# Performance work log

Measured on AMD Instinct MI355X. Metric: run time of the kernel, lower is better.

## Reference

```python
import jax, jax.numpy as jnp
import numpy as np

B, C, H, W = 4, 256, 64, 64
CK = C // 8  # query/key channels per OUT_RATIO=8


def setup_inputs() -> dict:
    key = jax.random.key(0)
    ks = jax.random.split(key, 8)
    s_in = 1.0 / np.sqrt(C)
    return {
        "x": jax.random.normal(ks[0], (B, C, H, W), dtype=jnp.float32),
        "Wq": jax.random.uniform(ks[1], (CK, C), jnp.float32, -s_in, s_in),
        "bq": jax.random.uniform(ks[2], (CK,), jnp.float32, -s_in, s_in),
        "Wk": jax.random.uniform(ks[3], (CK, C), jnp.float32, -s_in, s_in),
        "bk": jax.random.uniform(ks[4], (CK,), jnp.float32, -s_in, s_in),
        "Wv": jax.random.uniform(ks[5], (C, C), jnp.float32, -s_in, s_in),
        "bv": jax.random.uniform(ks[6], (C,), jnp.float32, -s_in, s_in),
        "gamma": jnp.zeros((1,), dtype=jnp.float32),
    }


def reference(x, Wq, bq, Wk, bk, Wv, bv, gamma):
    b, c, h, w = x.shape
    n = h * w
    xf = x.reshape(b, c, n)  # [B, C, N]
    # 1x1 convs are channel matmuls
    q = jnp.einsum('oc,bcn->bno', Wq, xf) + bq  # [B, N, CK]
    k = jnp.einsum('oc,bcn->bon', Wk, xf) + bk[None, :, None]  # [B, CK, N]
    v = jnp.einsum('oc,bcn->bon', Wv, xf) + bv[None, :, None]  # [B, C, N]
    energy = jnp.einsum('bno,bom->bnm', q, k)  # [B, N, N], unscaled
    attn = jax.nn.softmax(energy, axis=-1)
    out = jnp.einsum('bcm,bnm->bcn', v, attn)  # [B, C, N]
    out = out.reshape(b, c, h, w)
    return gamma[0] * out + x
```

## Files before the change

kernel.cpp:

```cpp
#include <hip/hip_runtime.h>
#include <math.h>


#define BB 4
#define CC 256
#define NN 4096
#define CKK 32
#define LOG2E 1.44269504f

typedef __attribute__((ext_vector_type(4))) float f32x4;
typedef __attribute__((ext_vector_type(16))) float f32x16;
typedef __attribute__((ext_vector_type(8))) short short8;
typedef __attribute__((ext_vector_type(4))) short short4v;

static __device__ __forceinline__ ushort f2bf(float f) {
    union { float f; unsigned u; } v; v.f = f;
    unsigned r = v.u + 0x7FFFu + ((v.u >> 16) & 1u);
    return (ushort)(r >> 16);
}
static __device__ __forceinline__ float bf2f(ushort h) {
    union { unsigned u; float f; } v; v.u = ((unsigned)h) << 16;
    return v.f;
}
static __device__ __forceinline__ unsigned pack2(float lo, float hi) {
    unsigned r;
    asm("v_cvt_pk_bf16_f32 %0, %1, %2" : "=v"(r) : "v"(lo), "v"(hi));
    return r;
}
static __device__ __forceinline__ float exp2fast(float x) {
    return __builtin_amdgcn_exp2f(x);
}

#define VSEL(chunk, c) (((chunk) * 1024) + ((((c) ^ (((chunk) >> 1) << 2))) << 2))

__global__ __launch_bounds__(256) void pack_w_kernel(
    const float* __restrict__ Wq, const float* __restrict__ bq,
    const float* __restrict__ Wk, const float* __restrict__ bk,
    const float* __restrict__ Wv, const float* __restrict__ bv,
    ushort* __restrict__ Wb, float* __restrict__ bias)
{
    const int o = blockIdx.x;
    const int c = threadIdx.x;
    const float* src; float bsc;
    if (o < 32)      { src = Wq + o * CC;        bsc = bq[o]; }
    else if (o < 64) { src = Wk + (o - 32) * CC; bsc = bk[o - 32]; }
    else             { src = Wv + (o - 64) * CC; bsc = bv[o - 64]; }
    Wb[o * CC + c] = f2bf(src[c]);
    if (c == 0) bias[o] = bsc;
}

__global__ __launch_bounds__(256) void xpose_kernel(
    const float* __restrict__ x, ushort* __restrict__ xT)
{
    __shared__ float t[32][33];
    const int b = blockIdx.z, c0 = blockIdx.y * 32, n0 = blockIdx.x * 32;
    const int tid = threadIdx.x;
    #pragma unroll
    for (int i = 0; i < 4; ++i) {
        int idx = tid + i * 256, rr = idx >> 5, nn = idx & 31;
        t[rr][nn] = x[((size_t)b * CC + c0 + rr) * NN + n0 + nn];
    }
    __syncthreads();
    #pragma unroll
    for (int i = 0; i < 4; ++i) {
        int idx = tid + i * 256, rr = idx >> 5, cc = idx & 31;
        xT[((size_t)b * NN + n0 + rr) * CC + c0 + cc] = f2bf(t[cc][rr]);
    }
}

__global__ __launch_bounds__(256) void qkv_mfma_kernel(
    const ushort* __restrict__ Wb, const float* __restrict__ bias,
    const ushort* __restrict__ xT,
    ushort* __restrict__ Q, ushort* __restrict__ Kt, ushort* __restrict__ V)
{
    const int b = blockIdx.y, n0 = blockIdx.x * 64;
    const int tid = threadIdx.x;
    const int w = tid >> 6, lane = tid & 63, l15 = lane & 15, q = lane >> 4;

    f32x4 acc[5][4];
    #pragma unroll
    for (int c5 = 0; c5 < 5; ++c5)
        #pragma unroll
        for (int nc = 0; nc < 4; ++nc) acc[c5][nc] = (f32x4)0.f;

    #pragma unroll
    for (int ks = 0; ks < 8; ++ks) {
        short8 af[5], bf[4];
        #pragma unroll
        for (int c5 = 0; c5 < 5; ++c5)
            af[c5] = *(const short8*)&Wb[(w * 80 + c5 * 16 + l15) * CC + ks * 32 + q * 8];
        #pragma unroll
        for (int nc = 0; nc < 4; ++nc)
            bf[nc] = *(const short8*)&xT[((size_t)b * NN + n0 + nc * 16 + l15) * CC + ks * 32 + q * 8];
        #pragma unroll
        for (int c5 = 0; c5 < 5; ++c5)
            #pragma unroll
            for (int nc = 0; nc < 4; ++nc)
                acc[c5][nc] = __builtin_amdgcn_mfma_f32_16x16x32_bf16(af[c5], bf[nc], acc[c5][nc], 0, 0, 0);
    }

    #pragma unroll
    for (int c5 = 0; c5 < 5; ++c5) {
        const int o0 = w * 80 + c5 * 16;
        float bia[4];
        #pragma unroll
        for (int r = 0; r < 4; ++r) bia[r] = bias[o0 + q * 4 + r];
        if (o0 >= 64) {
            #pragma unroll
            for (int nc = 0; nc < 4; ++nc)
                #pragma unroll
                for (int r = 0; r < 4; ++r)
                    V[((size_t)b * CC + o0 - 64 + q * 4 + r) * NN + n0 + nc * 16 + l15] =
                        f2bf(acc[c5][nc][r] + bia[r]);
        } else {
            ushort* dst = (o0 < 32) ? Q : Kt;
            const float sc = (o0 < 32) ? LOG2E : 1.0f;
            const int oo = (o0 & 31) + q * 4;
            #pragma unroll
            for (int nc = 0; nc < 4; ++nc) {
                short4v h;
                #pragma unroll
                for (int r = 0; r < 4; ++r) h[r] = (short)f2bf((acc[c5][nc][r] + bia[r]) * sc);
                *(short4v*)&dst[((size_t)b * NN + n0 + nc * 16 + l15) * CKK + oo] = h;
            }
        }
    }
}

__global__ __launch_bounds__(256, 2) void attn_mfma_kernel(
    const ushort* __restrict__ Q, const ushort* __restrict__ K,
    const ushort* __restrict__ V,
    ushort* __restrict__ Op, float* __restrict__ Mp, float* __restrict__ Lp,
    int G, int NSEG)
{
    __shared__ __align__(16) ushort vs2[2][8192];

    const int id = blockIdx.x;
    const int xcd = id & 7, ix = id >> 3;
    const int b = xcd >> 1;
    int g, row;
    if (G == 4) { g = ((xcd & 1) << 1) | (ix & 1); row = ix >> 1; }
    else        { g = xcd & 1;                     row = ix; }
    const int n0 = row * 128;

    const int tid = threadIdx.x;
    const int w = tid >> 6, lane = tid & 63;
    const int l31 = lane & 31, h2 = lane >> 5;
    const int n0w = n0 + w * 32;

    const size_t qrow = ((size_t)b * NN + n0w + l31) * CKK;
    short8 qB0 = *(const short8*)&Q[qrow + h2 * 8];
    short8 qB1 = *(const short8*)&Q[qrow + 16 + h2 * 8];

    f32x16 acc[8];
    #pragma unroll
    for (int cb = 0; cb < 8; ++cb) acc[cb] = (f32x16)0.f;
    float m_i = -3.0e38f, l_p = 0.f;

    const size_t kgb = (size_t)b * NN * CKK;
    const size_t vgb = (size_t)b * CC * NN;
    const int m_start = g * NSEG;
    const int NT = NSEG / 32;

    const int srow = tid >> 2, sseg = tid & 3;

    short8 kA0 = *(const short8*)&K[kgb + (size_t)(m_start + l31) * CKK + h2 * 8];
    short8 kA1 = *(const short8*)&K[kgb + (size_t)(m_start + l31) * CKK + 16 + h2 * 8];
    union { short8 v; short4v h[2]; } vr[4];
    #pragma unroll
    for (int i = 0; i < 4; ++i)
        vr[i].v = *(const short8*)&V[vgb + (size_t)(srow + i * 64) * NN + m_start + sseg * 8];
    #pragma unroll
    for (int i = 0; i < 4; ++i) {
        const int c = srow + i * 64;
        *(short4v*)&vs2[0][VSEL(2 * sseg,     c)] = vr[i].h[0];
        *(short4v*)&vs2[0][VSEL(2 * sseg + 1, c)] = vr[i].h[1];
    }
    __syncthreads();

    int cur = 0;
    for (int mt = 0; mt < NT; ++mt) {
        const bool more = (mt + 1 < NT);
        const int m0n = more ? m_start + (mt + 1) * 32 : m_start;

        f32x16 s = __builtin_amdgcn_mfma_f32_32x32x16_bf16(kA0, qB0, (f32x16)0.f, 0, 0, 0);
        s = __builtin_amdgcn_mfma_f32_32x32x16_bf16(kA1, qB1, s, 0, 0, 0);

        kA0 = *(const short8*)&K[kgb + (size_t)(m0n + l31) * CKK + h2 * 8];
        kA1 = *(const short8*)&K[kgb + (size_t)(m0n + l31) * CKK + 16 + h2 * 8];
        #pragma unroll
        for (int i = 0; i < 4; ++i)
            vr[i].v = *(const short8*)&V[vgb + (size_t)(srow + i * 64) * NN + m0n + sseg * 8];

        float mx = fmaxf(
            fmaxf(fmaxf(fmaxf(s[0], s[1]), fmaxf(s[2], s[3])),
                  fmaxf(fmaxf(s[4], s[5]), fmaxf(s[6], s[7]))),
            fmaxf(fmaxf(fmaxf(s[8], s[9]), fmaxf(s[10], s[11])),
                  fmaxf(fmaxf(s[12], s[13]), fmaxf(s[14], s[15]))));
        mx = fmaxf(mx, __shfl_xor(mx, 32));
        const bool resc = mx > m_i + 8.f;
        const float mn = resc ? mx : m_i;
        const float al = resc ? exp2fast(m_i - mx) : 1.f;
        float pp[16];
        #pragma unroll
        for (int r = 0; r < 16; ++r) pp[r] = exp2fast(s[r] - mn);
        float sum = ((pp[0] + pp[1]) + (pp[2] + pp[3])) + ((pp[4] + pp[5]) + (pp[6] + pp[7]))
                  + ((pp[8] + pp[9]) + (pp[10] + pp[11])) + ((pp[12] + pp[13]) + (pp[14] + pp[15]));
        l_p = l_p * al + sum;
        m_i = mn;
        if (__any(resc)) {
            #pragma unroll
            for (int cb = 0; cb < 8; ++cb) acc[cb] *= al;
        }

        union { unsigned u[8]; short8 v[2]; } P;
        #pragma unroll
        for (int g2 = 0; g2 < 8; ++g2) P.u[g2] = pack2(pp[2 * g2], pp[2 * g2 + 1]);

        __builtin_amdgcn_s_setprio(1);
        #pragma unroll
        for (int cb = 0; cb < 8; ++cb) {
            const int c = cb * 32 + l31;
            union { short4v h[2]; short8 v; } A0, A1;
            A0.h[0] = *(const short4v*)&vs2[cur][VSEL(h2,     c)];
            A0.h[1] = *(const short4v*)&vs2[cur][VSEL(2 + h2, c)];
            A1.h[0] = *(const short4v*)&vs2[cur][VSEL(4 + h2, c)];
            A1.h[1] = *(const short4v*)&vs2[cur][VSEL(6 + h2, c)];
            acc[cb] = __builtin_amdgcn_mfma_f32_32x32x16_bf16(A0.v, P.v[0], acc[cb], 0, 0, 0);
            acc[cb] = __builtin_amdgcn_mfma_f32_32x32x16_bf16(A1.v, P.v[1], acc[cb], 0, 0, 0);
        }
        __builtin_amdgcn_s_setprio(0);

        #pragma unroll
        for (int i = 0; i < 4; ++i) {
            const int c = srow + i * 64;
            *(short4v*)&vs2[cur ^ 1][VSEL(2 * sseg,     c)] = vr[i].h[0];
            *(short4v*)&vs2[cur ^ 1][VSEL(2 * sseg + 1, c)] = vr[i].h[1];
        }
        __syncthreads();
        cur ^= 1;
    }

    float l = l_p + __shfl_xor(l_p, 32);
    const float linv = 1.f / l;
    if (h2 == 0) {
        const size_t idx = (size_t)(g * BB + b) * NN + n0w + l31;
        Mp[idx] = m_i;
        Lp[idx] = l;
    }
    ushort* ob = Op + (size_t)(g * BB + b) * CC * NN;
    #pragma unroll
    for (int cb = 0; cb < 8; ++cb)
        #pragma unroll
        for (int r = 0; r < 16; ++r) {
            const int c = cb * 32 + (r & 3) + 8 * (r >> 2) + 4 * h2;
            ob[(size_t)c * NN + n0w + l31] = f2bf(acc[cb][r] * linv);
        }
}

template<int G>
__global__ __launch_bounds__(256) void combine_kernel(
    const ushort* __restrict__ Op, const float* __restrict__ Mp,
    const float* __restrict__ Lp, const float* __restrict__ x,
    const float* __restrict__ gamma, float* __restrict__ out)
{
    const int gid = blockIdx.x * 256 + threadIdx.x;
    const int grp   = gid & (NN / 8 - 1);
    const int rowid = gid >> 9;
    const int b = rowid >> 8;
    const int c = rowid & (CC - 1);
    const int n0 = grp * 8;

    f32x4 mp[G][2], lp[G][2];
    #pragma unroll
    for (int g = 0; g < G; ++g) {
        const size_t base = (size_t)(g * BB + b) * NN + n0;
        mp[g][0] = *(const f32x4*)&Mp[base];
        mp[g][1] = *(const f32x4*)&Mp[base + 4];
        lp[g][0] = *(const f32x4*)&Lp[base];
        lp[g][1] = *(const f32x4*)&Lp[base + 4];
    }
    float wgt[G][8];
    #pragma unroll
    for (int h = 0; h < 2; ++h) {
        #pragma unroll
        for (int j = 0; j < 4; ++j) {
            float M = -3.0e38f;
            #pragma unroll
            for (int g = 0; g < G; ++g) M = fmaxf(M, mp[g][h][j]);
            float ws = 0.f;
            #pragma unroll
            for (int g = 0; g < G; ++g) {
                const float wv = lp[g][h][j] * exp2fast(mp[g][h][j] - M);
                wgt[g][h * 4 + j] = wv;
                ws += wv;
            }
            const float inv = 1.f / ws;
            #pragma unroll
            for (int g = 0; g < G; ++g) wgt[g][h * 4 + j] *= inv;
        }
    }

    short8 opv[G];
    #pragma unroll
    for (int g = 0; g < G; ++g)
        opv[g] = *(const short8*)&Op[((size_t)(g * BB + b) * CC + c) * NN + n0];

    const size_t xbase = ((size_t)b * CC + c) * NN + n0;
    const f32x4 x0 = *(const f32x4*)&x[xbase];
    const f32x4 x1 = *(const f32x4*)&x[xbase + 4];
    const float gm = gamma[0];

    f32x4 o0, o1;
    #pragma unroll
    for (int j = 0; j < 4; ++j) {
        float a = 0.f, bsum = 0.f;
        #pragma unroll
        for (int g = 0; g < G; ++g) {
            a    += wgt[g][j]     * bf2f((ushort)opv[g][j]);
            bsum += wgt[g][4 + j] * bf2f((ushort)opv[g][4 + j]);
        }
        o0[j] = gm * a + x0[j];
        o1[j] = gm * bsum + x1[j];
    }
    *(f32x4*)&out[xbase]     = o0;
    *(f32x4*)&out[xbase + 4] = o1;
}

extern "C" void kernel_launch(void* const* d_in, const int* in_sizes, int n_in,
                              void* d_out, int out_size, void* d_ws, size_t ws_size,
                              hipStream_t stream) {
    const float* x     = (const float*)d_in[0];
    const float* Wq    = (const float*)d_in[1];
    const float* bq    = (const float*)d_in[2];
    const float* Wk    = (const float*)d_in[3];
    const float* bk    = (const float*)d_in[4];
    const float* Wv    = (const float*)d_in[5];
    const float* bv    = (const float*)d_in[6];
    const float* gamma = (const float*)d_in[7];
    float* out = (float*)d_out;

    char* p = (char*)d_ws;
    ushort* Wb   = (ushort*)(p);
    float*  bias = (float*) (p + 163840);
    ushort* xT   = (ushort*)(p + 165120);
    ushort* Qb   = (ushort*)(p + 8553728);
    ushort* Kb   = (ushort*)(p + 9602304);
    ushort* Vc   = (ushort*)(p + 10650880);
    float*  Mpb  = (float*) (p + 19039488);
    float*  Lpb  = (float*) (p + 19301632);
    ushort* Opb  = (ushort*)(p + 19563776);
    const int G = (ws_size >= (size_t)53118208) ? 4 : 2;

    pack_w_kernel<<<dim3(320), 256, 0, stream>>>(Wq, bq, Wk, bk, Wv, bv, Wb, bias);
    xpose_kernel<<<dim3(NN / 32, CC / 32, BB), 256, 0, stream>>>(x, xT);
    qkv_mfma_kernel<<<dim3(NN / 64, BB), 256, 0, stream>>>(Wb, bias, xT, Qb, Kb, Vc);
    attn_mfma_kernel<<<dim3(128 * G), 256, 0, stream>>>(Qb, Kb, Vc, Opb, Mpb, Lpb, G, NN / G);
    const int cblocks = BB * CC * (NN / 8) / 256;
    if (G == 4)
        combine_kernel<4><<<dim3(cblocks), 256, 0, stream>>>(Opb, Mpb, Lpb, x, gamma, out);
    else
        combine_kernel<2><<<dim3(cblocks), 256, 0, stream>>>(Opb, Mpb, Lpb, x, gamma, out);
}
```

Baseline: 97.24 us.

## Fuse transpose into QKV projection and software-pipeline QK^T in attention loop

Result: faster. 89.34 us (-8.1%).

```diff
diff --git a/kernel.cpp b/kernel.cpp
--- a/kernel.cpp
+++ b/kernel.cpp
@@ -30,8 +30,6 @@
 static __device__ __forceinline__ float exp2fast(float x) {
     return __builtin_amdgcn_exp2f(x);
 }
-
-#define VSEL(chunk, c) (((chunk) * 1024) + ((((c) ^ (((chunk) >> 1) << 2))) << 2))
 
 __global__ __launch_bounds__(256) void pack_w_kernel(
     const float* __restrict__ Wq, const float* __restrict__ bq,
@@ -49,28 +47,9 @@
     if (c == 0) bias[o] = bsc;
 }
 
-__global__ __launch_bounds__(256) void xpose_kernel(
-    const float* __restrict__ x, ushort* __restrict__ xT)
-{
-    __shared__ float t[32][33];
-    const int b = blockIdx.z, c0 = blockIdx.y * 32, n0 = blockIdx.x * 32;
-    const int tid = threadIdx.x;
-    #pragma unroll
-    for (int i = 0; i < 4; ++i) {
-        int idx = tid + i * 256, rr = idx >> 5, nn = idx & 31;
-        t[rr][nn] = x[((size_t)b * CC + c0 + rr) * NN + n0 + nn];
-    }
-    __syncthreads();
-    #pragma unroll
-    for (int i = 0; i < 4; ++i) {
-        int idx = tid + i * 256, rr = idx >> 5, cc = idx & 31;
-        xT[((size_t)b * NN + n0 + rr) * CC + c0 + cc] = f2bf(t[cc][rr]);
-    }
-}
-
 __global__ __launch_bounds__(256) void qkv_mfma_kernel(
     const ushort* __restrict__ Wb, const float* __restrict__ bias,
-    const ushort* __restrict__ xT,
+    const float* __restrict__ x,
     ushort* __restrict__ Q, ushort* __restrict__ Kt, ushort* __restrict__ V)
 {
     const int b = blockIdx.y, n0 = blockIdx.x * 64;
@@ -83,20 +62,28 @@
         #pragma unroll
         for (int nc = 0; nc < 4; ++nc) acc[c5][nc] = (f32x4)0.f;
 
+    const float* xb = x + (size_t)b * CC * NN + n0;
+
     #pragma unroll
     for (int ks = 0; ks < 8; ++ks) {
-        short8 af[5], bf[4];
+        short8 af[5];
         #pragma unroll
         for (int c5 = 0; c5 < 5; ++c5)
             af[c5] = *(const short8*)&Wb[(w * 80 + c5 * 16 + l15) * CC + ks * 32 + q * 8];
-        #pragma unroll
-        for (int nc = 0; nc < 4; ++nc)
-            bf[nc] = *(const short8*)&xT[((size_t)b * NN + n0 + nc * 16 + l15) * CC + ks * 32 + q * 8];
+        union { unsigned u[4]; short8 v; } bfu[4];
+        #pragma unroll
+        for (int nc = 0; nc < 4; ++nc) {
+            const float* xp = xb + (size_t)(ks * 32 + q * 8) * NN + nc * 16 + l15;
+            bfu[nc].u[0] = pack2(xp[0],          xp[(size_t)NN]);
+            bfu[nc].u[1] = pack2(xp[2 * (size_t)NN], xp[3 * (size_t)NN]);
+            bfu[nc].u[2] = pack2(xp[4 * (size_t)NN], xp[5 * (size_t)NN]);
+            bfu[nc].u[3] = pack2(xp[6 * (size_t)NN], xp[7 * (size_t)NN]);
+        }
         #pragma unroll
         for (int c5 = 0; c5 < 5; ++c5)
             #pragma unroll
             for (int nc = 0; nc < 4; ++nc)
-                acc[c5][nc] = __builtin_amdgcn_mfma_f32_16x16x32_bf16(af[c5], bf[nc], acc[c5][nc], 0, 0, 0);
+                acc[c5][nc] = __builtin_amdgcn_mfma_f32_16x16x32_bf16(af[c5], bfu[nc].v, acc[c5][nc], 0, 0, 0);
     }
 
     #pragma unroll
@@ -133,7 +120,7 @@
     ushort* __restrict__ Op, float* __restrict__ Mp, float* __restrict__ Lp,
     int G, int NSEG)
 {
-    __shared__ __align__(16) ushort vs2[2][8192];
+    __shared__ __align__(16) ushort vs2[2][4][256][8];
 
     const int id = blockIdx.x;
     const int xcd = id & 7, ix = id >> 3;
@@ -157,88 +144,96 @@
     for (int cb = 0; cb < 8; ++cb) acc[cb] = (f32x16)0.f;
     float m_i = -3.0e38f, l_p = 0.f;
 
-    const size_t kgb = (size_t)b * NN * CKK;
+    const ushort* Kb = K + (size_t)b * NN * CKK;
     const size_t vgb = (size_t)b * CC * NN;
     const int m_start = g * NSEG;
     const int NT = NSEG / 32;
 
     const int srow = tid >> 2, sseg = tid & 3;
-
-    short8 kA0 = *(const short8*)&K[kgb + (size_t)(m_start + l31) * CKK + h2 * 8];
-    short8 kA1 = *(const short8*)&K[kgb + (size_t)(m_start + l31) * CKK + 16 + h2 * 8];
+    const int kh2a = (sseg >> 1) << 1;
+    const int sslot = (sseg & 1) << 2;
+
+    short8 kA0 = *(const short8*)&Kb[(size_t)(m_start + l31) * CKK + h2 * 8];
+    short8 kA1 = *(const short8*)&Kb[(size_t)(m_start + l31) * CKK + 16 + h2 * 8];
     union { short8 v; short4v h[2]; } vr[4];
     #pragma unroll
     for (int i = 0; i < 4; ++i)
         vr[i].v = *(const short8*)&V[vgb + (size_t)(srow + i * 64) * NN + m_start + sseg * 8];
+    f32x16 s = __builtin_amdgcn_mfma_f32_32x32x16_bf16(kA0, qB0, (f32x16)0.f, 0, 0, 0);
+    s = __builtin_amdgcn_mfma_f32_32x32x16_bf16(kA1, qB1, s, 0, 0, 0);
+    const int mi1 = (NT > 1) ? m_start + 32 : m_start;
+    kA0 = *(const short8*)&Kb[(size_t)(mi1 + l31) * CKK + h2 * 8];
+    kA1 = *(const short8*)&Kb[(size_t)(mi1 + l31) * CKK + 16 + h2 * 8];
     #pragma unroll
     for (int i = 0; i < 4; ++i) {
         const int c = srow + i * 64;
-        *(short4v*)&vs2[0][VSEL(2 * sseg,     c)] = vr[i].h[0];
-        *(short4v*)&vs2[0][VSEL(2 * sseg + 1, c)] = vr[i].h[1];
-    }
+        *(short4v*)&vs2[0][kh2a + 0][c][sslot] = vr[i].h[0];
+        *(short4v*)&vs2[0][kh2a + 1][c][sslot] = vr[i].h[1];
+    }
+    #pragma unroll
+    for (int i = 0; i < 4; ++i)
+        vr[i].v = *(const short8*)&V[vgb + (size_t)(srow + i * 64) * NN + mi1 + sseg * 8];
     __syncthreads();
 
     int cur = 0;
     for (int mt = 0; mt < NT; ++mt) {
         const bool more = (mt + 1 < NT);
-        const int m0n = more ? m_start + (mt + 1) * 32 : m_start;
-
-        f32x16 s = __builtin_amdgcn_mfma_f32_32x32x16_bf16(kA0, qB0, (f32x16)0.f, 0, 0, 0);
-        s = __builtin_amdgcn_mfma_f32_32x32x16_bf16(kA1, qB1, s, 0, 0, 0);
-
-        kA0 = *(const short8*)&K[kgb + (size_t)(m0n + l31) * CKK + h2 * 8];
-        kA1 = *(const short8*)&K[kgb + (size_t)(m0n + l31) * CKK + 16 + h2 * 8];
-        #pragma unroll
-        for (int i = 0; i < 4; ++i)
-            vr[i].v = *(const short8*)&V[vgb + (size_t)(srow + i * 64) * NN + m0n + sseg * 8];
-
-        float mx = fmaxf(
-            fmaxf(fmaxf(fmaxf(s[0], s[1]), fmaxf(s[2], s[3])),
-                  fmaxf(fmaxf(s[4], s[5]), fmaxf(s[6], s[7]))),
-            fmaxf(fmaxf(fmaxf(s[8], s[9]), fmaxf(s[10], s[11])),
-                  fmaxf(fmaxf(s[12], s[13]), fmaxf(s[14], s[15]))));
+        const int mi2 = (mt + 2 < NT) ? m_start + (mt + 2) * 32 : m_start;
+
+        f32x16 sn = __builtin_amdgcn_mfma_f32_32x32x16_bf16(kA0, qB0, (f32x16)0.f, 0, 0, 0);
+        sn = __builtin_amdgcn_mfma_f32_32x32x16_bf16(kA1, qB1, sn, 0, 0, 0);
+        kA0 = *(const short8*)&Kb[(size_t)(mi2 + l31) * CKK + h2 * 8];
+        kA1 = *(const short8*)&Kb[(size_t)(mi2 + l31) * CKK + 16 + h2 * 8];
+
+        float t0 = fmaxf(fmaxf(s[0],  s[1]),  s[2]);
+        float t1 = fmaxf(fmaxf(s[3],  s[4]),  s[5]);
+        float t2 = fmaxf(fmaxf(s[6],  s[7]),  s[8]);
+        float t3 = fmaxf(fmaxf(s[9],  s[10]), s[11]);
+        float t4 = fmaxf(fmaxf(s[12], s[13]), s[14]);
+        float mx = fmaxf(fmaxf(fmaxf(t0, t1), t2), fmaxf(fmaxf(t3, t4), s[15]));
         mx = fmaxf(mx, __shfl_xor(mx, 32));
         const bool resc = mx > m_i + 8.f;
         const float mn = resc ? mx : m_i;
         const float al = resc ? exp2fast(m_i - mx) : 1.f;
-        float pp[16];
-        #pragma unroll
-        for (int r = 0; r < 16; ++r) pp[r] = exp2fast(s[r] - mn);
-        float sum = ((pp[0] + pp[1]) + (pp[2] + pp[3])) + ((pp[4] + pp[5]) + (pp[6] + pp[7]))
-                  + ((pp[8] + pp[9]) + (pp[10] + pp[11])) + ((pp[12] + pp[13]) + (pp[14] + pp[15]));
-        l_p = l_p * al + sum;
+        union { unsigned u[8]; short8 v[2]; } P;
+        float sum0 = 0.f, sum1 = 0.f;
+        #pragma unroll
+        for (int g2 = 0; g2 < 8; ++g2) {
+            const float plo = exp2fast(s[2 * g2]     - mn);
+            const float phi = exp2fast(s[2 * g2 + 1] - mn);
+            if (g2 & 1) sum1 += plo + phi; else sum0 += plo + phi;
+            P.u[g2] = pack2(plo, phi);
+        }
+        l_p = l_p * al + (sum0 + sum1);
         m_i = mn;
         if (__any(resc)) {
             #pragma unroll
             for (int cb = 0; cb < 8; ++cb) acc[cb] *= al;
         }
 
-        union { unsigned u[8]; short8 v[2]; } P;
-        #pragma unroll
-        for (int g2 = 0; g2 < 8; ++g2) P.u[g2] = pack2(pp[2 * g2], pp[2 * g2 + 1]);
-
         __builtin_amdgcn_s_setprio(1);
         #pragma unroll
         for (int cb = 0; cb < 8; ++cb) {
-            const int c = cb * 32 + l31;
-            union { short4v h[2]; short8 v; } A0, A1;
-            A0.h[0] = *(const short4v*)&vs2[cur][VSEL(h2,     c)];
-            A0.h[1] = *(const short4v*)&vs2[cur][VSEL(2 + h2, c)];
-            A1.h[0] = *(const short4v*)&vs2[cur][VSEL(4 + h2, c)];
-            A1.h[1] = *(const short4v*)&vs2[cur][VSEL(6 + h2, c)];
-            acc[cb] = __builtin_amdgcn_mfma_f32_32x32x16_bf16(A0.v, P.v[0], acc[cb], 0, 0, 0);
-            acc[cb] = __builtin_amdgcn_mfma_f32_32x32x16_bf16(A1.v, P.v[1], acc[cb], 0, 0, 0);
+            const short8 A0 = *(const short8*)&vs2[cur][h2][cb * 32 + l31][0];
+            const short8 A1 = *(const short8*)&vs2[cur][2 + h2][cb * 32 + l31][0];
+            acc[cb] = __builtin_amdgcn_mfma_f32_32x32x16_bf16(A0, P.v[0], acc[cb], 0, 0, 0);
+            acc[cb] = __builtin_amdgcn_mfma_f32_32x32x16_bf16(A1, P.v[1], acc[cb], 0, 0, 0);
         }
         __builtin_amdgcn_s_setprio(0);
 
-        #pragma unroll
-        for (int i = 0; i < 4; ++i) {
-            const int c = srow + i * 64;
-            *(short4v*)&vs2[cur ^ 1][VSEL(2 * sseg,     c)] = vr[i].h[0];
-            *(short4v*)&vs2[cur ^ 1][VSEL(2 * sseg + 1, c)] = vr[i].h[1];
-        }
-        __syncthreads();
-        cur ^= 1;
+        if (more) {
+            #pragma unroll
+            for (int i = 0; i < 4; ++i) {
+                const int c = srow + i * 64;
+                *(short4v*)&vs2[cur ^ 1][kh2a + 0][c][sslot] = vr[i].h[0];
+                *(short4v*)&vs2[cur ^ 1][kh2a + 1][c][sslot] = vr[i].h[1];
+            }
+            __syncthreads();
+            #pragma unroll
+            for (int i = 0; i < 4; ++i)
+                vr[i].v = *(const short8*)&V[vgb + (size_t)(srow + i * 64) * NN + mi2 + sseg * 8];
+        }
+        s = sn; cur ^= 1;
     }
 
     float l = l_p + __shfl_xor(l_p, 32);
@@ -343,18 +338,16 @@
     char* p = (char*)d_ws;
     ushort* Wb   = (ushort*)(p);
     float*  bias = (float*) (p + 163840);
-    ushort* xT   = (ushort*)(p + 165120);
-    ushort* Qb   = (ushort*)(p + 8553728);
-    ushort* Kb   = (ushort*)(p + 9602304);
-    ushort* Vc   = (ushort*)(p + 10650880);
-    float*  Mpb  = (float*) (p + 19039488);
-    float*  Lpb  = (float*) (p + 19301632);
-    ushort* Opb  = (ushort*)(p + 19563776);
-    const int G = (ws_size >= (size_t)53118208) ? 4 : 2;
+    ushort* Qb   = (ushort*)(p + 165120);
+    ushort* Kb   = (ushort*)(p + 1213696);
+    ushort* Vc   = (ushort*)(p + 2262272);
+    float*  Mpb  = (float*) (p + 10650880);
+    float*  Lpb  = (float*) (p + 10913024);
+    ushort* Opb  = (ushort*)(p + 11175168);
+    const int G = (ws_size >= (size_t)44729600) ? 4 : 2;
 
     pack_w_kernel<<<dim3(320), 256, 0, stream>>>(Wq, bq, Wk, bk, Wv, bv, Wb, bias);
-    xpose_kernel<<<dim3(NN / 32, CC / 32, BB), 256, 0, stream>>>(x, xT);
-    qkv_mfma_kernel<<<dim3(NN / 64, BB), 256, 0, stream>>>(Wb, bias, xT, Qb, Kb, Vc);
+    qkv_mfma_kernel<<<dim3(NN / 64, BB), 256, 0, stream>>>(Wb, bias, x, Qb, Kb, Vc);
     attn_mfma_kernel<<<dim3(128 * G), 256, 0, stream>>>(Qb, Kb, Vc, Opb, Mpb, Lpb, G, NN / G);
     const int cblocks = BB * CC * (NN / 8) / 256;
     if (G == 4)
```
